# Kernel tuning notes

Measured on AMD Instinct MI355X. Metric: run time of the kernel, lower is better.

The kernel has to match this reference:

```python
import jax, jax.numpy as jnp
import numpy as np

B, K, D = 16384, 32, 64
N_USERS, N_ENT, N_REL = 100000, 100000, 32
MAX_NORM = 1.0


def renorm(e):
    # emulate torch nn.Embedding(max_norm=1): rescale rows with norm > 1
    n = jnp.linalg.norm(e, axis=-1, keepdims=True)
    return e * jnp.minimum(1.0, MAX_NORM / jnp.maximum(n, 1e-7))


def setup_inputs() -> dict:
    key = jax.random.key(0)
    ks = jax.random.split(key, 9)
    return {
        "user_table": jax.random.normal(ks[0], (N_USERS, D), dtype=jnp.float32),
        "entity_table": jax.random.normal(ks[1], (N_ENT, D), dtype=jnp.float32),
        "relation_table": jax.random.normal(ks[2], (N_REL, D), dtype=jnp.float32),
        "W": jax.random.normal(ks[3], (D, D), dtype=jnp.float32) / np.sqrt(D),
        "b": jnp.zeros((D,), dtype=jnp.float32),
        "users": jax.random.randint(ks[4], (B,), 0, N_USERS),
        "items": jax.random.randint(ks[5], (B,), 0, N_ENT),
        "adj_entity": jax.random.randint(ks[6], (N_ENT, K), 0, N_ENT),
        "adj_relation": jax.random.randint(ks[7], (N_ENT, K), 0, N_REL),
    }


def reference(user_table, entity_table, relation_table, W, b,
              users, items, adj_entity, adj_relation):
    # neighbor id gather: [B, K]
    nbr_ent_ids = adj_entity[items]
    nbr_rel_ids = adj_relation[items]
    # embedding lookups with max_norm renorm
    user_emb = renorm(user_table[users])                 # [B, D]
    item_emb = renorm(entity_table[items])               # [B, D]
    nbr_ent = renorm(entity_table[nbr_ent_ids])          # [B, K, D]
    nbr_rel = renorm(relation_table[nbr_rel_ids])        # [B, K, D]
    # user-relation attention scores, softmax over neighbors
    scores = jnp.einsum('bd,bkd->bk', user_emb, nbr_rel)  # [B, K]
    attn = jax.nn.softmax(scores, axis=-1)
    # attention-weighted neighbor aggregation
    nbr_vec = jnp.einsum('bk,bkd->bd', attn, nbr_ent)     # [B, D]
    # sum aggregator + linear + relu (dropout omitted: eval-mode baseline)
    out = item_emb + nbr_vec
    out = jax.nn.relu(out @ W.T + b)
    return (user_emb, out)
```

## Files before the change

kernel.cpp:

```cpp
#include <hip/hip_runtime.h>
#include <math.h>

#define BB 16384
#define KK_N 32
#define DD 64
#define N_ENT 100000
#define N_REL 32

#define WS_REL_OFF_BYTES ((size_t)N_ENT * DD * 2)
#define WS_NEED_BYTES (WS_REL_OFF_BYTES + (size_t)N_REL * DD * 4)

#define PT_ENT  N_ENT
#define PT_USER (N_ENT + BB)
#define PT_ALL  (N_ENT + BB + N_REL)

__device__ __forceinline__ float dot4(float4 a, float4 b) {
    return a.x * b.x + a.y * b.y + a.z * b.z + a.w * b.w;
}

__device__ __forceinline__ float red16(float ss) {
    ss += __shfl_xor(ss, 1, 64);
    ss += __shfl_xor(ss, 2, 64);
    ss += __shfl_xor(ss, 4, 64);
    ss += __shfl_xor(ss, 8, 64);
    return ss;
}

__device__ __forceinline__ unsigned short f2bf(float x) {
    unsigned int u = __float_as_uint(x);
    u += 0x7fffu + ((u >> 16) & 1u);
    return (unsigned short)(u >> 16);
}

__device__ __forceinline__ float bf2f(unsigned short h) {
    return __uint_as_float(((unsigned int)h) << 16);
}

__device__ __forceinline__ float4 bf4(ushort4 h) {
    return make_float4(bf2f(h.x), bf2f(h.y), bf2f(h.z), bf2f(h.w));
}

__global__ __launch_bounds__(256) void precompute(
    const float* __restrict__ user_table,
    const float* __restrict__ entity_table,
    const float* __restrict__ relation_table,
    const int*   __restrict__ users,
    unsigned short* __restrict__ ent_bf,
    float* __restrict__ rel_ws,
    float* __restrict__ out_user)
{
    const int tid = threadIdx.x;
    const int gl  = tid & 15;
    const int t   = blockIdx.x * 16 + (tid >> 4);
    if (t >= PT_ALL) return;

    if (t < PT_ENT) {
        float4 v = *reinterpret_cast<const float4*>(&entity_table[(size_t)t * DD + gl * 4]);
        float ss = red16(dot4(v, v));
        float sc = fminf(1.0f, __builtin_amdgcn_rsqf(ss));
        ushort4 h;
        h.x = f2bf(v.x * sc); h.y = f2bf(v.y * sc);
        h.z = f2bf(v.z * sc); h.w = f2bf(v.w * sc);
        *reinterpret_cast<ushort4*>(&ent_bf[(size_t)t * DD + gl * 4]) = h;
    } else if (t < PT_USER) {
        int u = t - PT_ENT;
        int uid = users[u];
        float4 v = *reinterpret_cast<const float4*>(&user_table[(size_t)uid * DD + gl * 4]);
        float ss = red16(dot4(v, v));
        float sc = fminf(1.0f, __builtin_amdgcn_rsqf(ss));
        v.x *= sc; v.y *= sc; v.z *= sc; v.w *= sc;
        *reinterpret_cast<float4*>(&out_user[(size_t)u * DD + gl * 4]) = v;
    } else {
        int rr = t - PT_USER;
        float4 v = *reinterpret_cast<const float4*>(&relation_table[rr * DD + gl * 4]);
        float ss = red16(dot4(v, v));
        float sc = fminf(1.0f, __builtin_amdgcn_rsqf(ss));
        v.x *= sc; v.y *= sc; v.z *= sc; v.w *= sc;
        *reinterpret_cast<float4*>(&rel_ws[rr * DD + ((gl * 4) ^ ((rr & 15) << 2))]) = v;
    }
}

__global__ __launch_bounds__(256, 4) void kgcn_main(
    const unsigned short* __restrict__ ent_bf,
    const float* __restrict__ rel_ws,
    const float* __restrict__ W,
    const float* __restrict__ bias,
    const int*   __restrict__ items,
    const int*   __restrict__ adj_entity,
    const int*   __restrict__ adj_relation,
    const float* __restrict__ user_out,
    float* __restrict__ out_final)
{
    __shared__ __align__(16) float Wlds[64 * 64];
    __shared__ __align__(16) float RelLds[N_REL * DD];
    __shared__ __align__(16) float Vec[4][2][64];

    const int tid  = threadIdx.x;
    const int lane = tid & 63;
    const int wave = tid >> 6;
    const int grp  = lane >> 4;
    const int gl   = lane & 15;
    const int kk   = lane & 31;

    const int b0 = (blockIdx.x * 4 + wave) * 2;
    const int iid0 = __builtin_amdgcn_readfirstlane(items[b0]);
    const int iid1 = __builtin_amdgcn_readfirstlane(items[b0 + 1]);

    const int* abase = (lane < 32) ? adj_entity : adj_relation;
    const int adjv0 = abase[(size_t)iid0 * KK_N + kk];
    const int adjv1 = abase[(size_t)iid1 * KK_N + kk];

    int eid0[8], eid1[8];
    #pragma unroll
    for (int k0 = 0; k0 < 8; ++k0) {
        eid0[k0] = adj_entity[(size_t)iid0 * KK_N + k0 * 4 + grp];
        eid1[k0] = adj_entity[(size_t)iid1 * KK_N + k0 * 4 + grp];
    }
    ushort4 v0[8], v1[8];
    #pragma unroll
    for (int k0 = 0; k0 < 8; ++k0) {
        v0[k0] = *reinterpret_cast<const ushort4*>(&ent_bf[(size_t)eid0[k0] * DD + gl * 4]);
        v1[k0] = *reinterpret_cast<const ushort4*>(&ent_bf[(size_t)eid1[k0] * DD + gl * 4]);
    }
    float4 uv0 = *reinterpret_cast<const float4*>(&user_out[(size_t)b0 * DD + gl * 4]);
    float4 uv1 = *reinterpret_cast<const float4*>(&user_out[(size_t)(b0 + 1) * DD + gl * 4]);
    ushort4 it0 = *reinterpret_cast<const ushort4*>(&ent_bf[(size_t)iid0 * DD + gl * 4]);
    ushort4 it1 = *reinterpret_cast<const ushort4*>(&ent_bf[(size_t)iid1 * DD + gl * 4]);

    #pragma unroll
    for (int it = 0; it < 4; ++it) {
        int i = tid + it * 256;
        float4 w4 = reinterpret_cast<const float4*>(W)[i];
        int d = i >> 4;
        int j = (i & 15) * 4;
        *reinterpret_cast<float4*>(&Wlds[d * 64 + (j ^ ((d & 15) << 2))]) = w4;
    }
    #pragma unroll
    for (int it = 0; it < 2; ++it)
        reinterpret_cast<float4*>(RelLds)[tid + it * 256] =
            reinterpret_cast<const float4*>(rel_ws)[tid + it * 256];
    __syncthreads();

    if (lane < 16) {
        *reinterpret_cast<float4*>(&Vec[wave][0][gl * 4]) = uv0;
        *reinterpret_cast<float4*>(&Vec[wave][1][gl * 4]) = uv1;
    }

    const int rid0 = __shfl(adjv0, 32 + kk, 64);
    const int rid1 = __shfl(adjv1, 32 + kk, 64);
    const int sz0 = (rid0 & 15) << 2;
    const int sz1 = (rid1 & 15) << 2;
    const int dbase = (lane >> 5) * 32;
    float s0 = 0.0f, s1 = 0.0f;
    #pragma unroll
    for (int d0 = 0; d0 < 32; d0 += 4) {
        int d = dbase + d0;
        float4 q0 = *reinterpret_cast<const float4*>(&Vec[wave][0][d]);
        float4 r0 = *reinterpret_cast<const float4*>(&RelLds[rid0 * DD + (d ^ sz0)]);
        s0 += dot4(q0, r0);
        float4 q1 = *reinterpret_cast<const float4*>(&Vec[wave][1][d]);
        float4 r1 = *reinterpret_cast<const float4*>(&RelLds[rid1 * DD + (d ^ sz1)]);
        s1 += dot4(q1, r1);
    }
    s0 += __shfl_xor(s0, 32, 64);
    s1 += __shfl_xor(s1, 32, 64);

    float e0 = __expf(s0), e1 = __expf(s1);
    float sum0 = e0, sum1 = e1;
    #pragma unroll
    for (int m = 1; m < 32; m <<= 1) {
        sum0 += __shfl_xor(sum0, m, 64);
        sum1 += __shfl_xor(sum1, m, 64);
    }
    const float wk0 = e0 * __builtin_amdgcn_rcpf(sum0);
    const float wk1 = e1 * __builtin_amdgcn_rcpf(sum1);

    float4 acc0 = make_float4(0.f, 0.f, 0.f, 0.f);
    float4 acc1 = make_float4(0.f, 0.f, 0.f, 0.f);
    #pragma unroll
    for (int k0 = 0; k0 < 8; ++k0) {
        float c0 = __shfl(wk0, k0 * 4 + grp, 64);
        float4 f0 = bf4(v0[k0]);
        acc0.x = fmaf(c0, f0.x, acc0.x);
        acc0.y = fmaf(c0, f0.y, acc0.y);
        acc0.z = fmaf(c0, f0.z, acc0.z);
        acc0.w = fmaf(c0, f0.w, acc0.w);
        float c1 = __shfl(wk1, k0 * 4 + grp, 64);
        float4 f1 = bf4(v1[k0]);
        acc1.x = fmaf(c1, f1.x, acc1.x);
        acc1.y = fmaf(c1, f1.y, acc1.y);
        acc1.z = fmaf(c1, f1.z, acc1.z);
        acc1.w = fmaf(c1, f1.w, acc1.w);
    }
    #pragma unroll
    for (int m = 16; m < 64; m <<= 1) {
        acc0.x += __shfl_xor(acc0.x, m, 64);
        acc0.y += __shfl_xor(acc0.y, m, 64);
        acc0.z += __shfl_xor(acc0.z, m, 64);
        acc0.w += __shfl_xor(acc0.w, m, 64);
        acc1.x += __shfl_xor(acc1.x, m, 64);
        acc1.y += __shfl_xor(acc1.y, m, 64);
        acc1.z += __shfl_xor(acc1.z, m, 64);
        acc1.w += __shfl_xor(acc1.w, m, 64);
    }

    float4 f0 = bf4(it0), f1 = bf4(it1);
    float4 t0 = make_float4(f0.x + acc0.x, f0.y + acc0.y, f0.z + acc0.z, f0.w + acc0.w);
    float4 t1 = make_float4(f1.x + acc1.x, f1.y + acc1.y, f1.z + acc1.z, f1.w + acc1.w);
    if (lane < 16) {
        *reinterpret_cast<float4*>(&Vec[wave][0][gl * 4]) = t0;
        *reinterpret_cast<float4*>(&Vec[wave][1][gl * 4]) = t1;
    }

    const float bv = bias[lane];
    const float* wrow = &Wlds[lane * 64];
    const int twz = (lane & 15) << 2;
    float o0 = bv, o1 = bv;
    #pragma unroll
    for (int j0 = 0; j0 < 64; j0 += 4) {
        float4 wv = *reinterpret_cast<const float4*>(&wrow[j0 ^ twz]);
        float4 q0 = *reinterpret_cast<const float4*>(&Vec[wave][0][j0]);
        float4 q1 = *reinterpret_cast<const float4*>(&Vec[wave][1][j0]);
        o0 += dot4(q0, wv);
        o1 += dot4(q1, wv);
    }
    out_final[(size_t)b0 * DD + lane] = fmaxf(o0, 0.0f);
    out_final[(size_t)(b0 + 1) * DD + lane] = fmaxf(o1, 0.0f);
}

__global__ __launch_bounds__(256) void kgcn_fused(
    const float* __restrict__ user_table,
    const float* __restrict__ entity_table,
    const float* __restrict__ relation_table,
    const float* __restrict__ W,
    const float* __restrict__ bias,
    const int*   __restrict__ users,
    const int*   __restrict__ items,
    const int*   __restrict__ adj_entity,
    const int*   __restrict__ adj_relation,
    float* __restrict__ out_user,
    float* __restrict__ out_final)
{
    __shared__ __align__(16) float Wlds[64 * 64];
    __shared__ __align__(16) float RelLds[N_REL * DD];
    __shared__ __align__(16) float Vec[4][64];

    const int tid  = threadIdx.x;
    const int lane = tid & 63;
    const int wave = tid >> 6;
    const int grp  = lane >> 4;
    const int gl   = lane & 15;

    const int b = blockIdx.x * 4 + wave;
    const int uid = __builtin_amdgcn_readfirstlane(users[b]);
    const int iid = __builtin_amdgcn_readfirstlane(items[b]);

    const int kk = lane & 31;
    const int* abase = (lane < 32) ? adj_entity : adj_relation;
    const int adjv = abase[(size_t)iid * KK_N + kk];
    float4 uv = *reinterpret_cast<const float4*>(&user_table[(size_t)uid * DD + gl * 4]);
    float4 iv = *reinterpret_cast<const float4*>(&entity_table[(size_t)iid * DD + gl * 4]);

    #pragma unroll
    for (int it = 0; it < 4; ++it) {
        int i = tid + it * 256;
        float4 w4 = reinterpret_cast<const float4*>(W)[i];
        int d = i >> 4;
        int j = (i & 15) * 4;
        *reinterpret_cast<float4*>(&Wlds[d * 64 + (j ^ ((d & 15) << 2))]) = w4;
    }
    #pragma unroll
    for (int it = 0; it < 2; ++it) {
        int r = wave * 8 + it * 4 + grp;
        float4 vv = reinterpret_cast<const float4*>(relation_table)[r * 16 + gl];
        float ss = red16(dot4(vv, vv));
        float sc = fminf(1.0f, __builtin_amdgcn_rsqf(ss));
        vv.x *= sc; vv.y *= sc; vv.z *= sc; vv.w *= sc;
        *reinterpret_cast<float4*>(&RelLds[r * 64 + ((gl * 4) ^ ((r & 15) << 2))]) = vv;
    }

    float ssu = red16(dot4(uv, uv));
    float usc = fminf(1.0f, __builtin_amdgcn_rsqf(ssu));
    uv.x *= usc; uv.y *= usc; uv.z *= usc; uv.w *= usc;
    if (lane < 16)
        *reinterpret_cast<float4*>(&out_user[(size_t)b * DD + gl * 4]) = uv;

    int eid[8];
    #pragma unroll
    for (int k0 = 0; k0 < 8; ++k0)
        eid[k0] = __shfl(adjv, k0 * 4 + grp, 64);
    float4 v[8];
    #pragma unroll
    for (int k0 = 0; k0 < 8; ++k0)
        v[k0] = *reinterpret_cast<const float4*>(&entity_table[(size_t)eid[k0] * DD + gl * 4]);

    __syncthreads();
    if (lane < 16)
        *reinterpret_cast<float4*>(&Vec[wave][gl * 4]) = uv;

    const int rid = __shfl(adjv, 32 + kk, 64);
    const int srel = (rid & 15) << 2;
    const float* relrow = &RelLds[rid * 64];
    const int dbase = (lane >> 5) * 32;
    float score = 0.0f;
    #pragma unroll
    for (int d0 = 0; d0 < 32; d0 += 4) {
        int d = dbase + d0;
        float4 rv = *reinterpret_cast<const float4*>(&relrow[d ^ srel]);
        float4 tv = *reinterpret_cast<const float4*>(&Vec[wave][d]);
        score += dot4(tv, rv);
    }
    score += __shfl_xor(score, 32, 64);

    float mx = score;
    #pragma unroll
    for (int m = 1; m < 32; m <<= 1) mx = fmaxf(mx, __shfl_xor(mx, m, 64));
    float e = __expf(score - mx);
    float sum = e;
    #pragma unroll
    for (int m = 1; m < 32; m <<= 1) sum += __shfl_xor(sum, m, 64);
    const float attn = e * __builtin_amdgcn_rcpf(sum);

    float cc[8];
    #pragma unroll
    for (int k0 = 0; k0 < 8; ++k0)
        cc[k0] = __shfl(attn, k0 * 4 + grp, 64);

    float4 acc = make_float4(0.f, 0.f, 0.f, 0.f);
    #pragma unroll
    for (int k0 = 0; k0 < 8; ++k0) {
        float ss = red16(dot4(v[k0], v[k0]));
        float sc = fminf(1.0f, __builtin_amdgcn_rsqf(ss));
        float ck = cc[k0] * sc;
        acc.x = fmaf(ck, v[k0].x, acc.x);
        acc.y = fmaf(ck, v[k0].y, acc.y);
        acc.z = fmaf(ck, v[k0].z, acc.z);
        acc.w = fmaf(ck, v[k0].w, acc.w);
    }
    #pragma unroll
    for (int m = 16; m < 64; m <<= 1) {
        acc.x += __shfl_xor(acc.x, m, 64);
        acc.y += __shfl_xor(acc.y, m, 64);
        acc.z += __shfl_xor(acc.z, m, 64);
        acc.w += __shfl_xor(acc.w, m, 64);
    }

    float ssi = red16(dot4(iv, iv));
    float isc = fminf(1.0f, __builtin_amdgcn_rsqf(ssi));
    float4 tmp;
    tmp.x = fmaf(isc, iv.x, acc.x);
    tmp.y = fmaf(isc, iv.y, acc.y);
    tmp.z = fmaf(isc, iv.z, acc.z);
    tmp.w = fmaf(isc, iv.w, acc.w);
    if (lane < 16)
        *reinterpret_cast<float4*>(&Vec[wave][gl * 4]) = tmp;

    const float bv = bias[lane];
    const float* wrow = &Wlds[lane * 64];
    const int twz = (lane & 15) << 2;
    float o = bv;
    #pragma unroll
    for (int j0 = 0; j0 < 64; j0 += 4) {
        float4 wv = *reinterpret_cast<const float4*>(&wrow[j0 ^ twz]);
        float4 tv = *reinterpret_cast<const float4*>(&Vec[wave][j0]);
        o += dot4(tv, wv);
    }
    out_final[(size_t)b * DD + lane] = fmaxf(o, 0.0f);
}

extern "C" void kernel_launch(void* const* d_in, const int* in_sizes, int n_in,
                              void* d_out, int out_size, void* d_ws, size_t ws_size,
                              hipStream_t stream)
{
    const float* user_table     = (const float*)d_in[0];
    const float* entity_table   = (const float*)d_in[1];
    const float* relation_table = (const float*)d_in[2];
    const float* W              = (const float*)d_in[3];
    const float* bias           = (const float*)d_in[4];
    const int*   users          = (const int*)d_in[5];
    const int*   items          = (const int*)d_in[6];
    const int*   adj_entity     = (const int*)d_in[7];
    const int*   adj_relation   = (const int*)d_in[8];

    float* out_user  = (float*)d_out;
    float* out_final = (float*)d_out + (size_t)BB * DD;

    if (ws_size >= WS_NEED_BYTES) {
        unsigned short* ent_bf = (unsigned short*)d_ws;
        float* rel_ws = (float*)((char*)d_ws + WS_REL_OFF_BYTES);
        precompute<<<(PT_ALL + 15) / 16, 256, 0, stream>>>(
            user_table, entity_table, relation_table, users, ent_bf, rel_ws, out_user);
        kgcn_main<<<BB / 8, 256, 0, stream>>>(
            ent_bf, rel_ws, W, bias, items, adj_entity, adj_relation, out_user, out_final);
    } else {
        kgcn_fused<<<BB / 4, 256, 0, stream>>>(user_table, entity_table, relation_table,
                                               W, bias, users, items, adj_entity, adj_relation,
                                               out_user, out_final);
    }
}
```

Before: 30.18 us.

## Precompute per-user scores against all relations in the precompute kernel

Result: slower. 35.47 us (+17.5%).

```diff
diff --git a/kernel.cpp b/kernel.cpp
--- a/kernel.cpp
+++ b/kernel.cpp
@@ -7,17 +7,16 @@
 #define N_ENT 100000
 #define N_REL 32
 
-#define WS_REL_OFF_BYTES ((size_t)N_ENT * DD * 2)
-#define WS_NEED_BYTES (WS_REL_OFF_BYTES + (size_t)N_REL * DD * 4)
-
-#define PT_ENT  N_ENT
-#define PT_USER (N_ENT + BB)
-#define PT_ALL  (N_ENT + BB + N_REL)
+#define WS_P_OFF_BYTES ((size_t)N_ENT * DD * 2)
+#define WS_NEED_BYTES (WS_P_OFF_BYTES + (size_t)BB * KK_N * 4)
+
+#define NB_ENT ((N_ENT + 15) / 16)
+#define NB_UP  (BB / 64)
+#define GRID_PRE (NB_ENT + NB_UP)
 
 __device__ __forceinline__ float dot4(float4 a, float4 b) {
     return a.x * b.x + a.y * b.y + a.z * b.z + a.w * b.w;
 }
-
 __device__ __forceinline__ float red16(float ss) {
     ss += __shfl_xor(ss, 1, 64);
     ss += __shfl_xor(ss, 2, 64);
@@ -25,17 +24,14 @@
     ss += __shfl_xor(ss, 8, 64);
     return ss;
 }
-
 __device__ __forceinline__ unsigned short f2bf(float x) {
     unsigned int u = __float_as_uint(x);
     u += 0x7fffu + ((u >> 16) & 1u);
     return (unsigned short)(u >> 16);
 }
-
 __device__ __forceinline__ float bf2f(unsigned short h) {
     return __uint_as_float(((unsigned int)h) << 16);
 }
-
 __device__ __forceinline__ float4 bf4(ushort4 h) {
     return make_float4(bf2f(h.x), bf2f(h.y), bf2f(h.z), bf2f(h.w));
 }
@@ -46,15 +42,16 @@
     const float* __restrict__ relation_table,
     const int*   __restrict__ users,
     unsigned short* __restrict__ ent_bf,
-    float* __restrict__ rel_ws,
+    float* __restrict__ pbuf,
     float* __restrict__ out_user)
 {
     const int tid = threadIdx.x;
-    const int gl  = tid & 15;
-    const int t   = blockIdx.x * 16 + (tid >> 4);
-    if (t >= PT_ALL) return;
-
-    if (t < PT_ENT) {
+    const int blk = blockIdx.x;
+
+    if (blk < NB_ENT) {
+        const int gl = tid & 15;
+        const int t  = blk * 16 + (tid >> 4);
+        if (t >= N_ENT) return;
         float4 v = *reinterpret_cast<const float4*>(&entity_table[(size_t)t * DD + gl * 4]);
         float ss = red16(dot4(v, v));
         float sc = fminf(1.0f, __builtin_amdgcn_rsqf(ss));
@@ -62,37 +59,75 @@
         h.x = f2bf(v.x * sc); h.y = f2bf(v.y * sc);
         h.z = f2bf(v.z * sc); h.w = f2bf(v.w * sc);
         *reinterpret_cast<ushort4*>(&ent_bf[(size_t)t * DD + gl * 4]) = h;
-    } else if (t < PT_USER) {
-        int u = t - PT_ENT;
-        int uid = users[u];
-        float4 v = *reinterpret_cast<const float4*>(&user_table[(size_t)uid * DD + gl * 4]);
-        float ss = red16(dot4(v, v));
-        float sc = fminf(1.0f, __builtin_amdgcn_rsqf(ss));
-        v.x *= sc; v.y *= sc; v.z *= sc; v.w *= sc;
-        *reinterpret_cast<float4*>(&out_user[(size_t)u * DD + gl * 4]) = v;
-    } else {
-        int rr = t - PT_USER;
-        float4 v = *reinterpret_cast<const float4*>(&relation_table[rr * DD + gl * 4]);
-        float ss = red16(dot4(v, v));
-        float sc = fminf(1.0f, __builtin_amdgcn_rsqf(ss));
-        v.x *= sc; v.y *= sc; v.z *= sc; v.w *= sc;
-        *reinterpret_cast<float4*>(&rel_ws[rr * DD + ((gl * 4) ^ ((rr & 15) << 2))]) = v;
-    }
-}
-
-__global__ __launch_bounds__(256, 4) void kgcn_main(
+        return;
+    }
+
+    __shared__ __align__(16) float Tile[64 * DD];
+    const int lane = tid & 63;
+    const int wave = __builtin_amdgcn_readfirstlane(tid >> 6);
+    const int u0 = (blk - NB_ENT) * 64;
+
+    #pragma unroll
+    for (int it = 0; it < 4; ++it) {
+        int i = tid + it * 256;
+        int r = i >> 4, c4 = i & 15;
+        int uid = users[u0 + r];
+        float4 a = *reinterpret_cast<const float4*>(&user_table[(size_t)uid * DD + c4 * 4]);
+        *reinterpret_cast<float4*>(&Tile[r * DD + ((c4 * 4) ^ ((r & 15) << 2))]) = a;
+    }
+    __syncthreads();
+
+    float4 a[16];
+    float ss = 0.0f;
+    #pragma unroll
+    for (int q = 0; q < 16; ++q) {
+        a[q] = *reinterpret_cast<const float4*>(&Tile[lane * DD + ((q * 4) ^ ((lane & 15) << 2))]);
+        ss = fmaf(a[q].x, a[q].x, fmaf(a[q].y, a[q].y, fmaf(a[q].z, a[q].z, fmaf(a[q].w, a[q].w, ss))));
+    }
+    const float sc = fminf(1.0f, __builtin_amdgcn_rsqf(ss));
+
+    if (wave == 0) {
+        #pragma unroll
+        for (int q = 0; q < 16; ++q) {
+            float4 o = make_float4(a[q].x * sc, a[q].y * sc, a[q].z * sc, a[q].w * sc);
+            *reinterpret_cast<float4*>(&out_user[(size_t)(u0 + lane) * DD + q * 4]) = o;
+        }
+    }
+
+    float pr[8];
+    #pragma unroll
+    for (int rr = 0; rr < 8; ++rr) {
+        const int r = wave * 8 + rr;
+        const float* relr = &relation_table[(size_t)r * DD];
+        float dt = 0.0f, rss = 0.0f;
+        #pragma unroll
+        for (int q = 0; q < 16; ++q) {
+            float4 wv = *reinterpret_cast<const float4*>(&relr[q * 4]);
+            dt = fmaf(a[q].x, wv.x, dt);
+            dt = fmaf(a[q].y, wv.y, dt);
+            dt = fmaf(a[q].z, wv.z, dt);
+            dt = fmaf(a[q].w, wv.w, dt);
+            rss = fmaf(wv.x, wv.x, fmaf(wv.y, wv.y, fmaf(wv.z, wv.z, fmaf(wv.w, wv.w, rss))));
+        }
+        const float rsc = fminf(1.0f, __builtin_amdgcn_rsqf(rss));
+        pr[rr] = dt * rsc * sc;
+    }
+    float* prow = &pbuf[(size_t)(u0 + lane) * KK_N + wave * 8];
+    *reinterpret_cast<float4*>(prow)     = make_float4(pr[0], pr[1], pr[2], pr[3]);
+    *reinterpret_cast<float4*>(prow + 4) = make_float4(pr[4], pr[5], pr[6], pr[7]);
+}
+
+__global__ __launch_bounds__(256) void kgcn_main(
     const unsigned short* __restrict__ ent_bf,
-    const float* __restrict__ rel_ws,
+    const float* __restrict__ pbuf,
     const float* __restrict__ W,
     const float* __restrict__ bias,
     const int*   __restrict__ items,
     const int*   __restrict__ adj_entity,
     const int*   __restrict__ adj_relation,
-    const float* __restrict__ user_out,
     float* __restrict__ out_final)
 {
     __shared__ __align__(16) float Wlds[64 * 64];
-    __shared__ __align__(16) float RelLds[N_REL * DD];
     __shared__ __align__(16) float Vec[4][2][64];
 
     const int tid  = threadIdx.x;
@@ -106,9 +141,10 @@
     const int iid0 = __builtin_amdgcn_readfirstlane(items[b0]);
     const int iid1 = __builtin_amdgcn_readfirstlane(items[b0 + 1]);
 
-    const int* abase = (lane < 32) ? adj_entity : adj_relation;
-    const int adjv0 = abase[(size_t)iid0 * KK_N + kk];
-    const int adjv1 = abase[(size_t)iid1 * KK_N + kk];
+    const int rid0 = adj_relation[(size_t)iid0 * KK_N + kk];
+    const int rid1 = adj_relation[(size_t)iid1 * KK_N + kk];
+    const float s0 = pbuf[(size_t)b0 * KK_N + rid0];
+    const float s1 = pbuf[(size_t)(b0 + 1) * KK_N + rid1];
 
     int eid0[8], eid1[8];
     #pragma unroll
@@ -122,8 +158,6 @@
         v0[k0] = *reinterpret_cast<const ushort4*>(&ent_bf[(size_t)eid0[k0] * DD + gl * 4]);
         v1[k0] = *reinterpret_cast<const ushort4*>(&ent_bf[(size_t)eid1[k0] * DD + gl * 4]);
     }
-    float4 uv0 = *reinterpret_cast<const float4*>(&user_out[(size_t)b0 * DD + gl * 4]);
-    float4 uv1 = *reinterpret_cast<const float4*>(&user_out[(size_t)(b0 + 1) * DD + gl * 4]);
     ushort4 it0 = *reinterpret_cast<const ushort4*>(&ent_bf[(size_t)iid0 * DD + gl * 4]);
     ushort4 it1 = *reinterpret_cast<const ushort4*>(&ent_bf[(size_t)iid1 * DD + gl * 4]);
 
@@ -135,35 +169,7 @@
         int j = (i & 15) * 4;
         *reinterpret_cast<float4*>(&Wlds[d * 64 + (j ^ ((d & 15) << 2))]) = w4;
     }
-    #pragma unroll
-    for (int it = 0; it < 2; ++it)
-        reinterpret_cast<float4*>(RelLds)[tid + it * 256] =
-            reinterpret_cast<const float4*>(rel_ws)[tid + it * 256];
     __syncthreads();
-
-    if (lane < 16) {
-        *reinterpret_cast<float4*>(&Vec[wave][0][gl * 4]) = uv0;
-        *reinterpret_cast<float4*>(&Vec[wave][1][gl * 4]) = uv1;
-    }
-
-    const int rid0 = __shfl(adjv0, 32 + kk, 64);
-    const int rid1 = __shfl(adjv1, 32 + kk, 64);
-    const int sz0 = (rid0 & 15) << 2;
-    const int sz1 = (rid1 & 15) << 2;
-    const int dbase = (lane >> 5) * 32;
-    float s0 = 0.0f, s1 = 0.0f;
-    #pragma unroll
-    for (int d0 = 0; d0 < 32; d0 += 4) {
-        int d = dbase + d0;
-        float4 q0 = *reinterpret_cast<const float4*>(&Vec[wave][0][d]);
-        float4 r0 = *reinterpret_cast<const float4*>(&RelLds[rid0 * DD + (d ^ sz0)]);
-        s0 += dot4(q0, r0);
-        float4 q1 = *reinterpret_cast<const float4*>(&Vec[wave][1][d]);
-        float4 r1 = *reinterpret_cast<const float4*>(&RelLds[rid1 * DD + (d ^ sz1)]);
-        s1 += dot4(q1, r1);
-    }
-    s0 += __shfl_xor(s0, 32, 64);
-    s1 += __shfl_xor(s1, 32, 64);
 
     float e0 = __expf(s0), e1 = __expf(s1);
     float sum0 = e0, sum1 = e1;
@@ -387,11 +393,11 @@
 
     if (ws_size >= WS_NEED_BYTES) {
         unsigned short* ent_bf = (unsigned short*)d_ws;
-        float* rel_ws = (float*)((char*)d_ws + WS_REL_OFF_BYTES);
-        precompute<<<(PT_ALL + 15) / 16, 256, 0, stream>>>(
-            user_table, entity_table, relation_table, users, ent_bf, rel_ws, out_user);
-        kgcn_main<<<BB / 8, 256, 0, stream>>>(
-            ent_bf, rel_ws, W, bias, items, adj_entity, adj_relation, out_user, out_final);
+        float* pbuf = (float*)((char*)d_ws + WS_P_OFF_BYTES);
+        precompute<<<GRID_PRE, 256, 0, stream>>>(user_table, entity_table, relation_table,
+                                                 users, ent_bf, pbuf, out_user);
+        kgcn_main<<<BB / 8, 256, 0, stream>>>(ent_bf, pbuf, W, bias,
+                                              items, adj_entity, adj_relation, out_final);
     } else {
         kgcn_fused<<<BB / 4, 256, 0, stream>>>(user_table, entity_table, relation_table,
                                                W, bias, users, items, adj_entity, adj_relation,
```

## Use MFMA f16 for final linear layer and process four rows per wave

Applied to the files above, without the earlier changes.

Measured after the change: 31.62 us. +4.8%, slower.

```diff
diff --git a/kernel.cpp b/kernel.cpp
--- a/kernel.cpp
+++ b/kernel.cpp
@@ -14,10 +14,13 @@
 #define PT_USER (N_ENT + BB)
 #define PT_ALL  (N_ENT + BB + N_REL)
 
+typedef _Float16 f16x8 __attribute__((ext_vector_type(8)));
+typedef _Float16 f16x4 __attribute__((ext_vector_type(4)));
+typedef float    f32x4 __attribute__((ext_vector_type(4)));
+
 __device__ __forceinline__ float dot4(float4 a, float4 b) {
     return a.x * b.x + a.y * b.y + a.z * b.z + a.w * b.w;
 }
-
 __device__ __forceinline__ float red16(float ss) {
     ss += __shfl_xor(ss, 1, 64);
     ss += __shfl_xor(ss, 2, 64);
@@ -25,17 +28,14 @@
     ss += __shfl_xor(ss, 8, 64);
     return ss;
 }
-
 __device__ __forceinline__ unsigned short f2bf(float x) {
     unsigned int u = __float_as_uint(x);
     u += 0x7fffu + ((u >> 16) & 1u);
     return (unsigned short)(u >> 16);
 }
-
 __device__ __forceinline__ float bf2f(unsigned short h) {
     return __uint_as_float(((unsigned int)h) << 16);
 }
-
 __device__ __forceinline__ float4 bf4(ushort4 h) {
     return make_float4(bf2f(h.x), bf2f(h.y), bf2f(h.z), bf2f(h.w));
 }
@@ -80,7 +80,7 @@
     }
 }
 
-__global__ __launch_bounds__(256, 4) void kgcn_main(
+__global__ __launch_bounds__(256) void kgcn_main(
     const unsigned short* __restrict__ ent_bf,
     const float* __restrict__ rel_ws,
     const float* __restrict__ W,
@@ -91,9 +91,9 @@
     const float* __restrict__ user_out,
     float* __restrict__ out_final)
 {
-    __shared__ __align__(16) float Wlds[64 * 64];
     __shared__ __align__(16) float RelLds[N_REL * DD];
-    __shared__ __align__(16) float Vec[4][2][64];
+    __shared__ __align__(16) float Uv[4][4][64];
+    __shared__ __align__(16) _Float16 Th[16][72];
 
     const int tid  = threadIdx.x;
     const int lane = tid & 63;
@@ -102,39 +102,28 @@
     const int gl   = lane & 15;
     const int kk   = lane & 31;
 
-    const int b0 = (blockIdx.x * 4 + wave) * 2;
-    const int iid0 = __builtin_amdgcn_readfirstlane(items[b0]);
-    const int iid1 = __builtin_amdgcn_readfirstlane(items[b0 + 1]);
+    const int b0 = blockIdx.x * 16 + wave * 4;
+
+    int iid[4];
+    #pragma unroll
+    for (int e = 0; e < 4; ++e)
+        iid[e] = __builtin_amdgcn_readfirstlane(items[b0 + e]);
 
     const int* abase = (lane < 32) ? adj_entity : adj_relation;
-    const int adjv0 = abase[(size_t)iid0 * KK_N + kk];
-    const int adjv1 = abase[(size_t)iid1 * KK_N + kk];
-
-    int eid0[8], eid1[8];
-    #pragma unroll
-    for (int k0 = 0; k0 < 8; ++k0) {
-        eid0[k0] = adj_entity[(size_t)iid0 * KK_N + k0 * 4 + grp];
-        eid1[k0] = adj_entity[(size_t)iid1 * KK_N + k0 * 4 + grp];
-    }
-    ushort4 v0[8], v1[8];
-    #pragma unroll
-    for (int k0 = 0; k0 < 8; ++k0) {
-        v0[k0] = *reinterpret_cast<const ushort4*>(&ent_bf[(size_t)eid0[k0] * DD + gl * 4]);
-        v1[k0] = *reinterpret_cast<const ushort4*>(&ent_bf[(size_t)eid1[k0] * DD + gl * 4]);
-    }
-    float4 uv0 = *reinterpret_cast<const float4*>(&user_out[(size_t)b0 * DD + gl * 4]);
-    float4 uv1 = *reinterpret_cast<const float4*>(&user_out[(size_t)(b0 + 1) * DD + gl * 4]);
-    ushort4 it0 = *reinterpret_cast<const ushort4*>(&ent_bf[(size_t)iid0 * DD + gl * 4]);
-    ushort4 it1 = *reinterpret_cast<const ushort4*>(&ent_bf[(size_t)iid1 * DD + gl * 4]);
-
-    #pragma unroll
-    for (int it = 0; it < 4; ++it) {
-        int i = tid + it * 256;
-        float4 w4 = reinterpret_cast<const float4*>(W)[i];
-        int d = i >> 4;
-        int j = (i & 15) * 4;
-        *reinterpret_cast<float4*>(&Wlds[d * 64 + (j ^ ((d & 15) << 2))]) = w4;
-    }
+    int adjv[4];
+    #pragma unroll
+    for (int e = 0; e < 4; ++e)
+        adjv[e] = abase[(size_t)iid[e] * KK_N + kk];
+
+    float4 uv[4];
+    #pragma unroll
+    for (int e = 0; e < 4; ++e)
+        uv[e] = *reinterpret_cast<const float4*>(&user_out[(size_t)(b0 + e) * DD + gl * 4]);
+    ushort4 itm[4];
+    #pragma unroll
+    for (int e = 0; e < 4; ++e)
+        itm[e] = *reinterpret_cast<const ushort4*>(&ent_bf[(size_t)iid[e] * DD + gl * 4]);
+
     #pragma unroll
     for (int it = 0; it < 2; ++it)
         reinterpret_cast<float4*>(RelLds)[tid + it * 256] =
@@ -142,90 +131,100 @@
     __syncthreads();
 
     if (lane < 16) {
-        *reinterpret_cast<float4*>(&Vec[wave][0][gl * 4]) = uv0;
-        *reinterpret_cast<float4*>(&Vec[wave][1][gl * 4]) = uv1;
-    }
-
-    const int rid0 = __shfl(adjv0, 32 + kk, 64);
-    const int rid1 = __shfl(adjv1, 32 + kk, 64);
-    const int sz0 = (rid0 & 15) << 2;
-    const int sz1 = (rid1 & 15) << 2;
+        #pragma unroll
+        for (int e = 0; e < 4; ++e)
+            *reinterpret_cast<float4*>(&Uv[wave][e][gl * 4]) = uv[e];
+    }
+
     const int dbase = (lane >> 5) * 32;
-    float s0 = 0.0f, s1 = 0.0f;
-    #pragma unroll
-    for (int d0 = 0; d0 < 32; d0 += 4) {
-        int d = dbase + d0;
-        float4 q0 = *reinterpret_cast<const float4*>(&Vec[wave][0][d]);
-        float4 r0 = *reinterpret_cast<const float4*>(&RelLds[rid0 * DD + (d ^ sz0)]);
-        s0 += dot4(q0, r0);
-        float4 q1 = *reinterpret_cast<const float4*>(&Vec[wave][1][d]);
-        float4 r1 = *reinterpret_cast<const float4*>(&RelLds[rid1 * DD + (d ^ sz1)]);
-        s1 += dot4(q1, r1);
-    }
-    s0 += __shfl_xor(s0, 32, 64);
-    s1 += __shfl_xor(s1, 32, 64);
-
-    float e0 = __expf(s0), e1 = __expf(s1);
-    float sum0 = e0, sum1 = e1;
-    #pragma unroll
-    for (int m = 1; m < 32; m <<= 1) {
-        sum0 += __shfl_xor(sum0, m, 64);
-        sum1 += __shfl_xor(sum1, m, 64);
-    }
-    const float wk0 = e0 * __builtin_amdgcn_rcpf(sum0);
-    const float wk1 = e1 * __builtin_amdgcn_rcpf(sum1);
-
-    float4 acc0 = make_float4(0.f, 0.f, 0.f, 0.f);
-    float4 acc1 = make_float4(0.f, 0.f, 0.f, 0.f);
+    float wk[4];
+    #pragma unroll
+    for (int e = 0; e < 4; ++e) {
+        const int rid  = __shfl(adjv[e], 32 + kk, 64);
+        const int srel = (rid & 15) << 2;
+        const float* relrow = &RelLds[rid * DD];
+        float sc = 0.0f;
+        #pragma unroll
+        for (int d0 = 0; d0 < 32; d0 += 4) {
+            int d = dbase + d0;
+            float4 rv = *reinterpret_cast<const float4*>(&relrow[d ^ srel]);
+            float4 tv = *reinterpret_cast<const float4*>(&Uv[wave][e][d]);
+            sc += dot4(tv, rv);
+        }
+        sc += __shfl_xor(sc, 32, 64);
+        float ex = __expf(sc);
+        float sum = ex;
+        #pragma unroll
+        for (int m = 1; m < 32; m <<= 1) sum += __shfl_xor(sum, m, 64);
+        wk[e] = ex * __builtin_amdgcn_rcpf(sum);
+    }
+
+    float4 acc[4];
+    #pragma unroll
+    for (int e = 0; e < 4; ++e) acc[e] = make_float4(0.f, 0.f, 0.f, 0.f);
     #pragma unroll
     for (int k0 = 0; k0 < 8; ++k0) {
-        float c0 = __shfl(wk0, k0 * 4 + grp, 64);
-        float4 f0 = bf4(v0[k0]);
-        acc0.x = fmaf(c0, f0.x, acc0.x);
-        acc0.y = fmaf(c0, f0.y, acc0.y);
-        acc0.z = fmaf(c0, f0.z, acc0.z);
-        acc0.w = fmaf(c0, f0.w, acc0.w);
-        float c1 = __shfl(wk1, k0 * 4 + grp, 64);
-        float4 f1 = bf4(v1[k0]);
-        acc1.x = fmaf(c1, f1.x, acc1.x);
-        acc1.y = fmaf(c1, f1.y, acc1.y);
-        acc1.z = fmaf(c1, f1.z, acc1.z);
-        acc1.w = fmaf(c1, f1.w, acc1.w);
+        #pragma unroll
+        for (int e = 0; e < 4; ++e) {
+            int eid = adj_entity[(size_t)iid[e] * KK_N + k0 * 4 + grp];
+            ushort4 r = *reinterpret_cast<const ushort4*>(&ent_bf[(size_t)eid * DD + gl * 4]);
+            float c = __shfl(wk[e], k0 * 4 + grp, 64);
+            float4 f = bf4(r);
+            acc[e].x = fmaf(c, f.x, acc[e].x);
+            acc[e].y = fmaf(c, f.y, acc[e].y);
+            acc[e].z = fmaf(c, f.z, acc[e].z);
+            acc[e].w = fmaf(c, f.w, acc[e].w);
+        }
     }
     #pragma unroll
     for (int m = 16; m < 64; m <<= 1) {
-        acc0.x += __shfl_xor(acc0.x, m, 64);
-        acc0.y += __shfl_xor(acc0.y, m, 64);
-        acc0.z += __shfl_xor(acc0.z, m, 64);
-        acc0.w += __shfl_xor(acc0.w, m, 64);
-        acc1.x += __shfl_xor(acc1.x, m, 64);
-        acc1.y += __shfl_xor(acc1.y, m, 64);
-        acc1.z += __shfl_xor(acc1.z, m, 64);
-        acc1.w += __shfl_xor(acc1.w, m, 64);
-    }
-
-    float4 f0 = bf4(it0), f1 = bf4(it1);
-    float4 t0 = make_float4(f0.x + acc0.x, f0.y + acc0.y, f0.z + acc0.z, f0.w + acc0.w);
-    float4 t1 = make_float4(f1.x + acc1.x, f1.y + acc1.y, f1.z + acc1.z, f1.w + acc1.w);
+        #pragma unroll
+        for (int e = 0; e < 4; ++e) {
+            acc[e].x += __shfl_xor(acc[e].x, m, 64);
+            acc[e].y += __shfl_xor(acc[e].y, m, 64);
+            acc[e].z += __shfl_xor(acc[e].z, m, 64);
+            acc[e].w += __shfl_xor(acc[e].w, m, 64);
+        }
+    }
+
     if (lane < 16) {
-        *reinterpret_cast<float4*>(&Vec[wave][0][gl * 4]) = t0;
-        *reinterpret_cast<float4*>(&Vec[wave][1][gl * 4]) = t1;
-    }
-
-    const float bv = bias[lane];
-    const float* wrow = &Wlds[lane * 64];
-    const int twz = (lane & 15) << 2;
-    float o0 = bv, o1 = bv;
-    #pragma unroll
-    for (int j0 = 0; j0 < 64; j0 += 4) {
-        float4 wv = *reinterpret_cast<const float4*>(&wrow[j0 ^ twz]);
-        float4 q0 = *reinterpret_cast<const float4*>(&Vec[wave][0][j0]);
-        float4 q1 = *reinterpret_cast<const float4*>(&Vec[wave][1][j0]);
-        o0 += dot4(q0, wv);
-        o1 += dot4(q1, wv);
-    }
-    out_final[(size_t)b0 * DD + lane] = fmaxf(o0, 0.0f);
-    out_final[(size_t)(b0 + 1) * DD + lane] = fmaxf(o1, 0.0f);
+        #pragma unroll
+        for (int e = 0; e < 4; ++e) {
+            float4 f = bf4(itm[e]);
+            f16x4 h;
+            h[0] = (_Float16)(f.x + acc[e].x);
+            h[1] = (_Float16)(f.y + acc[e].y);
+            h[2] = (_Float16)(f.z + acc[e].z);
+            h[3] = (_Float16)(f.w + acc[e].w);
+            *reinterpret_cast<f16x4*>(&Th[wave * 4 + e][gl * 4]) = h;
+        }
+    }
+    __syncthreads();
+
+    const int n0  = wave * 16;
+    const int row = lane & 15;
+    const int kg  = (lane >> 4) * 8;
+    f32x4 d = {0.f, 0.f, 0.f, 0.f};
+    #pragma unroll
+    for (int kb = 0; kb < 64; kb += 32) {
+        f16x8 a = *reinterpret_cast<const f16x8*>(&Th[row][kb + kg]);
+        const float* wr = &W[(size_t)(n0 + row) * DD + kb + kg];
+        float4 w0 = *reinterpret_cast<const float4*>(wr);
+        float4 w1 = *reinterpret_cast<const float4*>(wr + 4);
+        f16x8 bfr;
+        bfr[0] = (_Float16)w0.x; bfr[1] = (_Float16)w0.y;
+        bfr[2] = (_Float16)w0.z; bfr[3] = (_Float16)w0.w;
+        bfr[4] = (_Float16)w1.x; bfr[5] = (_Float16)w1.y;
+        bfr[6] = (_Float16)w1.z; bfr[7] = (_Float16)w1.w;
+        d = __builtin_amdgcn_mfma_f32_16x16x32_f16(a, bfr, d, 0, 0, 0);
+    }
+    const float bcol = bias[n0 + row];
+    #pragma unroll
+    for (int r = 0; r < 4; ++r) {
+        int orow = (lane >> 4) * 4 + r;
+        int gb = blockIdx.x * 16 + orow;
+        out_final[(size_t)gb * DD + n0 + row] = fmaxf(d[r] + bcol, 0.0f);
+    }
 }
 
 __global__ __launch_bounds__(256) void kgcn_fused(
@@ -390,7 +389,7 @@
         float* rel_ws = (float*)((char*)d_ws + WS_REL_OFF_BYTES);
         precompute<<<(PT_ALL + 15) / 16, 256, 0, stream>>>(
             user_table, entity_table, relation_table, users, ent_bf, rel_ws, out_user);
-        kgcn_main<<<BB / 8, 256, 0, stream>>>(
+        kgcn_main<<<BB / 16, 256, 0, stream>>>(
             ent_bf, rel_ws, W, bias, items, adj_entity, adj_relation, out_user, out_final);
     } else {
         kgcn_fused<<<BB / 4, 256, 0, stream>>>(user_table, entity_table, relation_table,
```

## Compute final linear layer with fp16 MFMA and drop W staging in LDS

Applied to the files above, without the earlier changes.

After: 30.65 us. Within noise of the previous version (+1.6%).

```diff
diff --git a/kernel.cpp b/kernel.cpp
--- a/kernel.cpp
+++ b/kernel.cpp
@@ -14,10 +14,13 @@
 #define PT_USER (N_ENT + BB)
 #define PT_ALL  (N_ENT + BB + N_REL)
 
+typedef _Float16 f16x8 __attribute__((ext_vector_type(8)));
+typedef _Float16 f16x4 __attribute__((ext_vector_type(4)));
+typedef float    f32x4 __attribute__((ext_vector_type(4)));
+
 __device__ __forceinline__ float dot4(float4 a, float4 b) {
     return a.x * b.x + a.y * b.y + a.z * b.z + a.w * b.w;
 }
-
 __device__ __forceinline__ float red16(float ss) {
     ss += __shfl_xor(ss, 1, 64);
     ss += __shfl_xor(ss, 2, 64);
@@ -25,17 +28,14 @@
     ss += __shfl_xor(ss, 8, 64);
     return ss;
 }
-
 __device__ __forceinline__ unsigned short f2bf(float x) {
     unsigned int u = __float_as_uint(x);
     u += 0x7fffu + ((u >> 16) & 1u);
     return (unsigned short)(u >> 16);
 }
-
 __device__ __forceinline__ float bf2f(unsigned short h) {
     return __uint_as_float(((unsigned int)h) << 16);
 }
-
 __device__ __forceinline__ float4 bf4(ushort4 h) {
     return make_float4(bf2f(h.x), bf2f(h.y), bf2f(h.z), bf2f(h.w));
 }
@@ -80,7 +80,7 @@
     }
 }
 
-__global__ __launch_bounds__(256, 4) void kgcn_main(
+__global__ __launch_bounds__(256) void kgcn_main(
     const unsigned short* __restrict__ ent_bf,
     const float* __restrict__ rel_ws,
     const float* __restrict__ W,
@@ -91,9 +91,9 @@
     const float* __restrict__ user_out,
     float* __restrict__ out_final)
 {
-    __shared__ __align__(16) float Wlds[64 * 64];
     __shared__ __align__(16) float RelLds[N_REL * DD];
-    __shared__ __align__(16) float Vec[4][2][64];
+    __shared__ __align__(16) float Uv[4][2][64];
+    __shared__ __align__(16) _Float16 Th[16][72];
 
     const int tid  = threadIdx.x;
     const int lane = tid & 63;
@@ -128,22 +128,14 @@
     ushort4 it1 = *reinterpret_cast<const ushort4*>(&ent_bf[(size_t)iid1 * DD + gl * 4]);
 
     #pragma unroll
-    for (int it = 0; it < 4; ++it) {
-        int i = tid + it * 256;
-        float4 w4 = reinterpret_cast<const float4*>(W)[i];
-        int d = i >> 4;
-        int j = (i & 15) * 4;
-        *reinterpret_cast<float4*>(&Wlds[d * 64 + (j ^ ((d & 15) << 2))]) = w4;
-    }
-    #pragma unroll
     for (int it = 0; it < 2; ++it)
         reinterpret_cast<float4*>(RelLds)[tid + it * 256] =
             reinterpret_cast<const float4*>(rel_ws)[tid + it * 256];
     __syncthreads();
 
     if (lane < 16) {
-        *reinterpret_cast<float4*>(&Vec[wave][0][gl * 4]) = uv0;
-        *reinterpret_cast<float4*>(&Vec[wave][1][gl * 4]) = uv1;
+        *reinterpret_cast<float4*>(&Uv[wave][0][gl * 4]) = uv0;
+        *reinterpret_cast<float4*>(&Uv[wave][1][gl * 4]) = uv1;
     }
 
     const int rid0 = __shfl(adjv0, 32 + kk, 64);
@@ -155,10 +147,10 @@
     #pragma unroll
     for (int d0 = 0; d0 < 32; d0 += 4) {
         int d = dbase + d0;
-        float4 q0 = *reinterpret_cast<const float4*>(&Vec[wave][0][d]);
+        float4 q0 = *reinterpret_cast<const float4*>(&Uv[wave][0][d]);
         float4 r0 = *reinterpret_cast<const float4*>(&RelLds[rid0 * DD + (d ^ sz0)]);
         s0 += dot4(q0, r0);
-        float4 q1 = *reinterpret_cast<const float4*>(&Vec[wave][1][d]);
+        float4 q1 = *reinterpret_cast<const float4*>(&Uv[wave][1][d]);
         float4 r1 = *reinterpret_cast<const float4*>(&RelLds[rid1 * DD + (d ^ sz1)]);
         s1 += dot4(q1, r1);
     }
@@ -204,28 +196,48 @@
         acc1.w += __shfl_xor(acc1.w, m, 64);
     }
 
-    float4 f0 = bf4(it0), f1 = bf4(it1);
-    float4 t0 = make_float4(f0.x + acc0.x, f0.y + acc0.y, f0.z + acc0.z, f0.w + acc0.w);
-    float4 t1 = make_float4(f1.x + acc1.x, f1.y + acc1.y, f1.z + acc1.z, f1.w + acc1.w);
     if (lane < 16) {
-        *reinterpret_cast<float4*>(&Vec[wave][0][gl * 4]) = t0;
-        *reinterpret_cast<float4*>(&Vec[wave][1][gl * 4]) = t1;
-    }
-
-    const float bv = bias[lane];
-    const float* wrow = &Wlds[lane * 64];
-    const int twz = (lane & 15) << 2;
-    float o0 = bv, o1 = bv;
-    #pragma unroll
-    for (int j0 = 0; j0 < 64; j0 += 4) {
-        float4 wv = *reinterpret_cast<const float4*>(&wrow[j0 ^ twz]);
-        float4 q0 = *reinterpret_cast<const float4*>(&Vec[wave][0][j0]);
-        float4 q1 = *reinterpret_cast<const float4*>(&Vec[wave][1][j0]);
-        o0 += dot4(q0, wv);
-        o1 += dot4(q1, wv);
-    }
-    out_final[(size_t)b0 * DD + lane] = fmaxf(o0, 0.0f);
-    out_final[(size_t)(b0 + 1) * DD + lane] = fmaxf(o1, 0.0f);
+        float4 f0 = bf4(it0), f1 = bf4(it1);
+        f16x4 h0, h1;
+        h0[0] = (_Float16)(f0.x + acc0.x);
+        h0[1] = (_Float16)(f0.y + acc0.y);
+        h0[2] = (_Float16)(f0.z + acc0.z);
+        h0[3] = (_Float16)(f0.w + acc0.w);
+        h1[0] = (_Float16)(f1.x + acc1.x);
+        h1[1] = (_Float16)(f1.y + acc1.y);
+        h1[2] = (_Float16)(f1.z + acc1.z);
+        h1[3] = (_Float16)(f1.w + acc1.w);
+        *reinterpret_cast<f16x4*>(&Th[wave * 2 + 0][gl * 4]) = h0;
+        *reinterpret_cast<f16x4*>(&Th[wave * 2 + 1][gl * 4]) = h1;
+    }
+    __syncthreads();
+
+    const int n0  = wave * 16;
+    const int row = lane & 15;
+    const int kg  = (lane >> 4) * 8;
+    f32x4 d = {0.f, 0.f, 0.f, 0.f};
+    #pragma unroll
+    for (int kb = 0; kb < 64; kb += 32) {
+        f16x8 a = *reinterpret_cast<const f16x8*>(&Th[row][kb + kg]);
+        const float* wr = &W[(size_t)(n0 + row) * DD + kb + kg];
+        float4 w0 = *reinterpret_cast<const float4*>(wr);
+        float4 w1 = *reinterpret_cast<const float4*>(wr + 4);
+        f16x8 bfr;
+        bfr[0] = (_Float16)w0.x; bfr[1] = (_Float16)w0.y;
+        bfr[2] = (_Float16)w0.z; bfr[3] = (_Float16)w0.w;
+        bfr[4] = (_Float16)w1.x; bfr[5] = (_Float16)w1.y;
+        bfr[6] = (_Float16)w1.z; bfr[7] = (_Float16)w1.w;
+        d = __builtin_amdgcn_mfma_f32_16x16x32_f16(a, bfr, d, 0, 0, 0);
+    }
+    const float bcol = bias[n0 + row];
+    if (lane < 32) {
+        #pragma unroll
+        for (int r = 0; r < 4; ++r) {
+            int orow = (lane >> 4) * 4 + r;
+            int gb = blockIdx.x * 8 + orow;
+            out_final[(size_t)gb * DD + n0 + row] = fmaxf(d[r] + bcol, 0.0f);
+        }
+    }
 }
 
 __global__ __launch_bounds__(256) void kgcn_fused(
```
